# Kernel optimization log

Hardware: AMD Instinct MI355X
Metric: run time of the kernel (lower is better)

Reference implementation:

```python
import jax, jax.numpy as jnp
import numpy as np

B, S, H, D = 4, 1024, 16, 128
E = H * D  # 2048
TOTAL = B * S
NUM_SLOTS = 2 * TOTAL


def setup_inputs() -> dict:
    key = jax.random.key(0)
    k1, k2, k3, k4, k5 = jax.random.split(key, 5)
    return {
        "hidden_states": jax.random.normal(k1, (TOTAL, E), dtype=jnp.float32) * 0.02,
        "c_attn_w": jax.random.normal(k2, (E, 3 * E), dtype=jnp.float32) * 0.02,
        "c_attn_b": jax.random.normal(k3, (3 * E,), dtype=jnp.float32) * 0.02,
        "c_proj_w": jax.random.normal(k4, (E, E), dtype=jnp.float32) * 0.02,
        "c_proj_b": jax.random.normal(k5, (E,), dtype=jnp.float32) * 0.02,
        "key_cache": jnp.zeros((NUM_SLOTS, H, D), dtype=jnp.float32),
        "value_cache": jnp.zeros((NUM_SLOTS, H, D), dtype=jnp.float32),
        "slots": jnp.arange(TOTAL, dtype=jnp.int32),
        "seq_len": S,
    }


def reference(hidden_states, c_attn_w, c_attn_b, c_proj_w, c_proj_b,
              key_cache, value_cache, slots, seq_len):
    total, embed = hidden_states.shape
    n_heads, head_dim = key_cache.shape[1], key_cache.shape[2]
    b = total // seq_len

    # fused QKV projection (fan_in_fan_out: y = x @ W + b)
    qkv = hidden_states @ c_attn_w + c_attn_b            # [total, 3E]
    qkv = qkv.reshape(total, 3, n_heads, head_dim)
    q, k, v = qkv[:, 0], qkv[:, 1], qkv[:, 2]

    # paged_attention.reshape_and_cache: scatter new k/v into the paged cache
    key_cache = key_cache.at[slots].set(k)
    value_cache = value_cache.at[slots].set(v)
    # prefill attention reads current tokens' k/v (gathered back from cache)
    k = key_cache[slots]
    v = value_cache[slots]

    # varlen causal flash attention over b equal-length sequences
    qb = q.reshape(b, seq_len, n_heads, head_dim)
    kb = k.reshape(b, seq_len, n_heads, head_dim)
    vb = v.reshape(b, seq_len, n_heads, head_dim)
    scale = jnp.asarray(head_dim, qb.dtype) ** -0.5       # softmax_scale
    scores = jnp.einsum("bqhd,bkhd->bhqk", qb, kb) * scale
    causal = jnp.tril(jnp.ones((seq_len, seq_len), dtype=bool))
    scores = jnp.where(causal, scores, jnp.finfo(scores.dtype).min)
    attn = jax.nn.softmax(scores, axis=-1)
    ctx = jnp.einsum("bhqk,bkhd->bqhd", attn, vb)
    ctx = ctx.reshape(total, embed)

    # output projection (fan_in_fan_out row-parallel linear)
    out = ctx @ c_proj_w + c_proj_b
    return out
```

## Files before the change

kernel.cpp:

```cpp
#include <hip/hip_runtime.h>
#include <stdint.h>

typedef __bf16 bf16x8 __attribute__((ext_vector_type(8)));
typedef float  f32x4  __attribute__((ext_vector_type(4)));

#define DEV static __device__ __forceinline__

DEV unsigned short f2bf(float x) {
    union { float f; unsigned int u; } v; v.f = x;
    unsigned int r = v.u + 0x7FFFu + ((v.u >> 16) & 1u);
    return (unsigned short)(r >> 16);
}

DEV void gl_lds16(const void* g, void* l) {
    __builtin_amdgcn_global_load_lds(
        (__attribute__((address_space(1))) void*)(g),
        (__attribute__((address_space(3))) void*)(l), 16, 0, 0);
}

DEV f32x4 zero4() { f32x4 z; z[0]=0.f; z[1]=0.f; z[2]=0.f; z[3]=0.f; return z; }

__global__ void k_cvt_bf16(const float* __restrict__ in, unsigned short* __restrict__ out, int n) {
    int i = (blockIdx.x * blockDim.x + threadIdx.x) * 4;
    int stride = gridDim.x * blockDim.x * 4;
    for (; i < n; i += stride) {
        float4 f = *(const float4*)(in + i);
        ushort4 o;
        o.x = f2bf(f.x); o.y = f2bf(f.y); o.z = f2bf(f.z); o.w = f2bf(f.w);
        *(ushort4*)(out + i) = o;
    }
}

__global__ void k_transpose_bf16(const float* __restrict__ in, unsigned short* __restrict__ out,
                                 int K, int N) {
    __shared__ float tile[32][33];
    int n0 = blockIdx.x * 32, k0 = blockIdx.y * 32;
    int tx = threadIdx.x, ty = threadIdx.y;
    #pragma unroll
    for (int i = 0; i < 4; i++)
        tile[ty + i*8][tx] = in[(size_t)(k0 + ty + i*8) * N + n0 + tx];
    __syncthreads();
    #pragma unroll
    for (int i = 0; i < 4; i++)
        out[(size_t)(n0 + ty + i*8) * K + k0 + tx] = f2bf(tile[tx][ty + i*8]);
}

template<int MODE>
__launch_bounds__(256, 4)
__global__ void k_gemm(const unsigned short* __restrict__ A,
                       const unsigned short* __restrict__ BT,
                       const float* __restrict__ bias,
                       float* __restrict__ outp,
                       unsigned short* __restrict__ q_buf,
                       unsigned short* __restrict__ k_buf,
                       unsigned short* __restrict__ vt_buf,
                       int M, int N, int K) {
    __shared__ __align__(16) uint4 As[128*8];
    __shared__ __align__(16) uint4 Bs[128*8];

    const int t = threadIdx.x;
    const int wave = t >> 6, lane = t & 63, quad = lane >> 4, l15 = lane & 15;
    const int wm = wave & 1, wn = wave >> 1;
    const int bm = blockIdx.x, bn = blockIdx.y;

    f32x4 acc[4][4];
    #pragma unroll
    for (int i = 0; i < 4; i++)
        #pragma unroll
        for (int j = 0; j < 4; j++) acc[i][j] = zero4();

    int rS[4], gS[4];
    #pragma unroll
    for (int p = 0; p < 4; p++) {
        int c = p*4 + wave;
        int s = c*64 + lane;
        int r = s >> 3;
        rS[p] = r; gS[p] = (lane & 7) ^ (r & 7);
    }
    const unsigned short* Abase = A  + (size_t)(bm*128) * K;
    const unsigned short* Bbase = BT + (size_t)(bn*128) * K;

    const int kiters = K >> 6;
    for (int kk = 0; kk < kiters; kk++) {
        const int k0 = kk * 64;
        __syncthreads();
        #pragma unroll
        for (int p = 0; p < 4; p++) {
            int c = p*4 + wave;
            gl_lds16(Abase + (size_t)rS[p]*K + k0 + gS[p]*8, &As[c*64]);
            gl_lds16(Bbase + (size_t)rS[p]*K + k0 + gS[p]*8, &Bs[c*64]);
        }
        __syncthreads();
        #pragma unroll
        for (int ks = 0; ks < 2; ks++) {
            bf16x8 af[4], bfr[4];
            #pragma unroll
            for (int mt = 0; mt < 4; mt++) {
                int row = wm*64 + mt*16 + l15;
                int g = (ks*4 + quad) ^ (row & 7);
                af[mt] = __builtin_bit_cast(bf16x8, As[row*8 + g]);
            }
            #pragma unroll
            for (int nt = 0; nt < 4; nt++) {
                int row = wn*64 + nt*16 + l15;
                int g = (ks*4 + quad) ^ (row & 7);
                bfr[nt] = __builtin_bit_cast(bf16x8, Bs[row*8 + g]);
            }
            #pragma unroll
            for (int mt = 0; mt < 4; mt++)
                #pragma unroll
                for (int nt = 0; nt < 4; nt++)
                    acc[mt][nt] = __builtin_amdgcn_mfma_f32_16x16x32_bf16(
                        af[mt], bfr[nt], acc[mt][nt], 0, 0, 0);
        }
    }

    if (MODE == 1) {
        #pragma unroll
        for (int nt = 0; nt < 4; nt++) {
            int n = bn*128 + wn*64 + nt*16 + l15;
            float bv = bias[n];
            #pragma unroll
            for (int mt = 0; mt < 4; mt++) {
                int m = bm*128 + wm*64 + mt*16 + quad*4;
                #pragma unroll
                for (int r = 0; r < 4; r++)
                    outp[(size_t)(m + r) * N + n] = acc[mt][nt][r] + bv;
            }
        }
    } else {
        const int nglob = bn * 128;
        const int seg = nglob >> 11;
        const int cn_base = (nglob & 2047) + wn*64;
        if (seg < 2) {
            unsigned short* dst = (seg == 0) ? q_buf : k_buf;
            const float scl = (seg == 0) ? 0.08838834764831845f : 1.0f;
            #pragma unroll
            for (int nt = 0; nt < 4; nt++) {
                int cn = cn_base + nt*16 + l15;
                float bv = bias[nglob + wn*64 + nt*16 + l15];
                #pragma unroll
                for (int mt = 0; mt < 4; mt++) {
                    int tt = bm*128 + wm*64 + mt*16 + quad*4;
                    #pragma unroll
                    for (int r = 0; r < 4; r++)
                        dst[(size_t)(tt + r) * 2048 + cn] = f2bf((acc[mt][nt][r] + bv) * scl);
                }
            }
        } else {
            #pragma unroll
            for (int nt = 0; nt < 4; nt++) {
                int cn = cn_base + nt*16 + l15;
                int h = cn >> 7, d = cn & 127;
                float bv = bias[nglob + wn*64 + nt*16 + l15];
                #pragma unroll
                for (int mt = 0; mt < 4; mt++) {
                    int tt = bm*128 + wm*64 + mt*16 + quad*4;
                    int b = tt >> 10, s = tt & 1023;
                    ushort4 pk;
                    pk.x = f2bf(acc[mt][nt][0] + bv);
                    pk.y = f2bf(acc[mt][nt][1] + bv);
                    pk.z = f2bf(acc[mt][nt][2] + bv);
                    pk.w = f2bf(acc[mt][nt][3] + bv);
                    *(ushort4*)(vt_buf + ((size_t)((b*16 + h)*128 + d) * 1024 + s)) = pk;
                }
            }
        }
    }
}

#define ATTN_ITEMS 512
__launch_bounds__(256, 2)
__global__ void k_attn(const unsigned short* __restrict__ q_buf,
                       const unsigned short* __restrict__ k_buf,
                       const unsigned short* __restrict__ vt_buf,
                       unsigned short* __restrict__ ctx_buf,
                       int* __restrict__ counter) {
    __shared__ __align__(16) uint4 Ks[64*16];
    __shared__ __align__(16) uint4 Vs[128*8];
    __shared__ __align__(16) unsigned short Pl[4][32*64];
    __shared__ int sh_item;

    const int t = threadIdx.x;
    const int wave = t >> 6, lane = t & 63, quad = lane >> 4, l15 = lane & 15;

    for (;;) {
        if (t == 0) sh_item = atomicAdd(counter, 1);
        __syncthreads();
        const int u = sh_item;
        if (u >= ATTN_ITEMS) break;
        const int qt = 7 - (u >> 6);
        const int bh = u & 63;
        const int b = bh >> 4, h = bh & 15;

        bf16x8 qf[2][4];
        #pragma unroll
        for (int rt = 0; rt < 2; rt++) {
            const size_t qoff = (size_t)(b*1024 + qt*128 + wave*32 + rt*16 + l15) * 2048 + h*128;
            #pragma unroll
            for (int ks = 0; ks < 4; ks++)
                qf[rt][ks] = __builtin_bit_cast(bf16x8, *(const uint4*)(q_buf + qoff + ks*32 + quad*8));
        }

        f32x4 ctx[2][8];
        #pragma unroll
        for (int rt = 0; rt < 2; rt++)
            #pragma unroll
            for (int i = 0; i < 8; i++) ctx[rt][i] = zero4();
        float l_run[2][4];
        #pragma unroll
        for (int rt = 0; rt < 2; rt++)
            #pragma unroll
            for (int r = 0; r < 4; r++) l_run[rt][r] = 0.f;

        const size_t kbase = (size_t)b * 1024 * 2048 + h*128;
        const size_t vbase = (size_t)(b*16 + h) * 131072;
        const int row0 = qt*128 + wave*32;

        const int kiters = 2*qt + 2;
        for (int kt = 0; kt < kiters; kt++) {
            __syncthreads();
            #pragma unroll
            for (int p = 0; p < 4; p++) {
                int c = p*4 + wave;
                {
                    int s = c*64 + lane;
                    int r = s >> 4;
                    int g = (s & 15) ^ (r & 15);
                    gl_lds16(k_buf + kbase + (size_t)(kt*64 + r) * 2048 + g*8, &Ks[c*64]);
                }
                {
                    int s = c*64 + lane;
                    int r = s >> 3;
                    int g = (lane & 7) ^ (r & 7);
                    gl_lds16(vt_buf + vbase + (size_t)r * 1024 + kt*64 + g*8, &Vs[c*64]);
                }
            }
            __syncthreads();

            if (kt*64 > row0 + 31) continue;
            const bool needmask = (kt*64 + 63 > row0);

            #pragma unroll
            for (int rt = 0; rt < 2; rt++) {
                f32x4 sacc[4];
                #pragma unroll
                for (int nt = 0; nt < 4; nt++) sacc[nt] = zero4();
                #pragma unroll
                for (int ks = 0; ks < 4; ks++)
                    #pragma unroll
                    for (int nt = 0; nt < 4; nt++) {
                        int key = nt*16 + l15;
                        int g = (ks*4 + quad) ^ (key & 15);
                        bf16x8 kf = __builtin_bit_cast(bf16x8, Ks[key*16 + g]);
                        sacc[nt] = __builtin_amdgcn_mfma_f32_16x16x32_bf16(qf[rt][ks], kf, sacc[nt], 0, 0, 0);
                    }

                float pv[4][4];
                if (needmask) {
                    #pragma unroll
                    for (int nt = 0; nt < 4; nt++)
                        #pragma unroll
                        for (int r = 0; r < 4; r++) {
                            bool masked = (kt*64 + nt*16 + l15 > row0 + rt*16 + quad*4 + r);
                            pv[nt][r] = masked ? 0.f : __expf(sacc[nt][r]);
                        }
                } else {
                    #pragma unroll
                    for (int nt = 0; nt < 4; nt++)
                        #pragma unroll
                        for (int r = 0; r < 4; r++)
                            pv[nt][r] = __expf(sacc[nt][r]);
                }
                #pragma unroll
                for (int r = 0; r < 4; r++)
                    l_run[rt][r] += (pv[0][r] + pv[1][r]) + (pv[2][r] + pv[3][r]);

                #pragma unroll
                for (int nt = 0; nt < 4; nt++)
                    #pragma unroll
                    for (int r = 0; r < 4; r++) {
                        int row = rt*16 + quad*4 + r;
                        int col = nt*16 + l15;
                        int gc = (col >> 3) ^ (row & 7);
                        Pl[wave][row*64 + gc*8 + (col & 7)] = f2bf(pv[nt][r]);
                    }
            }
            __asm__ volatile("s_waitcnt lgkmcnt(0)" ::: "memory");

            #pragma unroll
            for (int rt = 0; rt < 2; rt++)
                #pragma unroll
                for (int ks = 0; ks < 2; ks++) {
                    int row = rt*16 + l15;
                    int gp = (ks*4 + quad) ^ (row & 7);
                    bf16x8 pa = __builtin_bit_cast(bf16x8, *(const uint4*)&Pl[wave][row*64 + gp*8]);
                    #pragma unroll
                    for (int dt = 0; dt < 8; dt++) {
                        int drow = dt*16 + l15;
                        int gv = (ks*4 + quad) ^ (drow & 7);
                        bf16x8 vf = __builtin_bit_cast(bf16x8, Vs[drow*8 + gv]);
                        ctx[rt][dt] = __builtin_amdgcn_mfma_f32_16x16x32_bf16(pa, vf, ctx[rt][dt], 0, 0, 0);
                    }
                }
        }

        #pragma unroll
        for (int rt = 0; rt < 2; rt++) {
            float inv[4];
            #pragma unroll
            for (int r = 0; r < 4; r++) {
                float l = l_run[rt][r];
                l += __shfl_xor(l, 1);
                l += __shfl_xor(l, 2);
                l += __shfl_xor(l, 4);
                l += __shfl_xor(l, 8);
                inv[r] = 1.0f / l;
            }
            const int tt0 = b*1024 + qt*128 + wave*32 + rt*16 + quad*4;
            #pragma unroll
            for (int dt = 0; dt < 8; dt++)
                #pragma unroll
                for (int r = 0; r < 4; r++)
                    ctx_buf[(size_t)(tt0 + r) * 2048 + h*128 + dt*16 + l15] = f2bf(ctx[rt][dt][r] * inv[r]);
        }
    }
}

extern "C" void kernel_launch(void* const* d_in, const int* in_sizes, int n_in,
                              void* d_out, int out_size, void* d_ws, size_t ws_size,
                              hipStream_t stream) {
    const float* hs    = (const float*)d_in[0];
    const float* wqkv  = (const float*)d_in[1];
    const float* bqkv  = (const float*)d_in[2];
    const float* wproj = (const float*)d_in[3];
    const float* bproj = (const float*)d_in[4];

    char* ws = (char*)d_ws;
    unsigned short* hs_bf   = (unsigned short*)(ws);
    unsigned short* wqkvT   = (unsigned short*)(ws + 16777216ull);
    unsigned short* wprojT  = (unsigned short*)(ws + 41943040ull);
    unsigned short* q_buf   = (unsigned short*)(ws + 50331648ull);
    unsigned short* k_buf   = (unsigned short*)(ws + 67108864ull);
    unsigned short* vt_buf  = (unsigned short*)(ws + 83886080ull);
    unsigned short* ctx_buf = (unsigned short*)(ws + 100663296ull);
    int* counter = (int*)ws;

    k_cvt_bf16<<<2048, 256, 0, stream>>>(hs, hs_bf, 4096 * 2048);
    k_transpose_bf16<<<dim3(6144/32, 2048/32), dim3(32, 8), 0, stream>>>(wqkv, wqkvT, 2048, 6144);
    k_transpose_bf16<<<dim3(2048/32, 2048/32), dim3(32, 8), 0, stream>>>(wproj, wprojT, 2048, 2048);

    k_gemm<0><<<dim3(32, 48), 256, 0, stream>>>(hs_bf, wqkvT, bqkv, nullptr,
                                                q_buf, k_buf, vt_buf, 4096, 6144, 2048);
    hipMemsetAsync(counter, 0, 4, stream);
    k_attn<<<dim3(448), 256, 0, stream>>>(q_buf, k_buf, vt_buf, ctx_buf, counter);
    k_gemm<1><<<dim3(32, 16), 256, 0, stream>>>(ctx_buf, wprojT, bproj, (float*)d_out,
                                                nullptr, nullptr, nullptr, 4096, 2048, 2048);
}
```

Before: 392.3 us.

## Split projection GEMM into 64-row tiles and interleave attention MFMAs

```diff
diff --git a/kernel.cpp b/kernel.cpp
--- a/kernel.cpp
+++ b/kernel.cpp
@@ -45,16 +45,14 @@
         out[(size_t)(n0 + ty + i*8) * K + k0 + tx] = f2bf(tile[tx][ty + i*8]);
 }
 
-template<int MODE>
 __launch_bounds__(256, 4)
-__global__ void k_gemm(const unsigned short* __restrict__ A,
-                       const unsigned short* __restrict__ BT,
-                       const float* __restrict__ bias,
-                       float* __restrict__ outp,
-                       unsigned short* __restrict__ q_buf,
-                       unsigned short* __restrict__ k_buf,
-                       unsigned short* __restrict__ vt_buf,
-                       int M, int N, int K) {
+__global__ void k_gemm_qkv(const unsigned short* __restrict__ A,
+                           const unsigned short* __restrict__ BT,
+                           const float* __restrict__ bias,
+                           unsigned short* __restrict__ q_buf,
+                           unsigned short* __restrict__ k_buf,
+                           unsigned short* __restrict__ vt_buf,
+                           int K) {
     __shared__ __align__(16) uint4 As[128*8];
     __shared__ __align__(16) uint4 Bs[128*8];
 
@@ -115,62 +113,128 @@
         }
     }
 
-    if (MODE == 1) {
+    const int nglob = bn * 128;
+    const int seg = nglob >> 11;
+    const int cn_base = (nglob & 2047) + wn*64;
+    if (seg < 2) {
+        unsigned short* dst = (seg == 0) ? q_buf : k_buf;
+        const float scl = (seg == 0) ? 0.08838834764831845f : 1.0f;
         #pragma unroll
         for (int nt = 0; nt < 4; nt++) {
-            int n = bn*128 + wn*64 + nt*16 + l15;
-            float bv = bias[n];
+            int cn = cn_base + nt*16 + l15;
+            float bv = bias[nglob + wn*64 + nt*16 + l15];
             #pragma unroll
             for (int mt = 0; mt < 4; mt++) {
-                int m = bm*128 + wm*64 + mt*16 + quad*4;
+                int tt = bm*128 + wm*64 + mt*16 + quad*4;
                 #pragma unroll
                 for (int r = 0; r < 4; r++)
-                    outp[(size_t)(m + r) * N + n] = acc[mt][nt][r] + bv;
+                    dst[(size_t)(tt + r) * 2048 + cn] = f2bf((acc[mt][nt][r] + bv) * scl);
             }
         }
     } else {
-        const int nglob = bn * 128;
-        const int seg = nglob >> 11;
-        const int cn_base = (nglob & 2047) + wn*64;
-        if (seg < 2) {
-            unsigned short* dst = (seg == 0) ? q_buf : k_buf;
-            const float scl = (seg == 0) ? 0.08838834764831845f : 1.0f;
+        #pragma unroll
+        for (int nt = 0; nt < 4; nt++) {
+            int cn = cn_base + nt*16 + l15;
+            int h = cn >> 7, d = cn & 127;
+            float bv = bias[nglob + wn*64 + nt*16 + l15];
+            #pragma unroll
+            for (int mt = 0; mt < 4; mt++) {
+                int tt = bm*128 + wm*64 + mt*16 + quad*4;
+                int b = tt >> 10, s = tt & 1023;
+                ushort4 pk;
+                pk.x = f2bf(acc[mt][nt][0] + bv);
+                pk.y = f2bf(acc[mt][nt][1] + bv);
+                pk.z = f2bf(acc[mt][nt][2] + bv);
+                pk.w = f2bf(acc[mt][nt][3] + bv);
+                *(ushort4*)(vt_buf + ((size_t)((b*16 + h)*128 + d) * 1024 + s)) = pk;
+            }
+        }
+    }
+}
+
+__launch_bounds__(256, 4)
+__global__ void k_gemm_proj(const unsigned short* __restrict__ A,
+                            const unsigned short* __restrict__ BT,
+                            const float* __restrict__ bias,
+                            float* __restrict__ outp,
+                            int N, int K) {
+    __shared__ __align__(16) uint4 As[64*8];
+    __shared__ __align__(16) uint4 Bs[128*8];
+
+    const int t = threadIdx.x;
+    const int wave = t >> 6, lane = t & 63, quad = lane >> 4, l15 = lane & 15;
+    const int wm = wave & 1, wn = wave >> 1;
+    const int bm = blockIdx.x, bn = blockIdx.y;
+
+    f32x4 acc[2][4];
+    #pragma unroll
+    for (int i = 0; i < 2; i++)
+        #pragma unroll
+        for (int j = 0; j < 4; j++) acc[i][j] = zero4();
+
+    int rS[4], gS[4];
+    #pragma unroll
+    for (int p = 0; p < 4; p++) {
+        int c = p*4 + wave;
+        int s = c*64 + lane;
+        int r = s >> 3;
+        rS[p] = r; gS[p] = (lane & 7) ^ (r & 7);
+    }
+    const unsigned short* Abase = A  + (size_t)(bm*64)  * K;
+    const unsigned short* Bbase = BT + (size_t)(bn*128) * K;
+
+    const int kiters = K >> 6;
+    for (int kk = 0; kk < kiters; kk++) {
+        const int k0 = kk * 64;
+        __syncthreads();
+        #pragma unroll
+        for (int p = 0; p < 4; p++) {
+            int c = p*4 + wave;
+            if (p < 2)
+                gl_lds16(Abase + (size_t)rS[p]*K + k0 + gS[p]*8, &As[c*64]);
+            gl_lds16(Bbase + (size_t)rS[p]*K + k0 + gS[p]*8, &Bs[c*64]);
+        }
+        __syncthreads();
+        #pragma unroll
+        for (int ks = 0; ks < 2; ks++) {
+            bf16x8 af[2], bfr[4];
+            #pragma unroll
+            for (int mt = 0; mt < 2; mt++) {
+                int row = wm*32 + mt*16 + l15;
+                int g = (ks*4 + quad) ^ (row & 7);
+                af[mt] = __builtin_bit_cast(bf16x8, As[row*8 + g]);
+            }
             #pragma unroll
             for (int nt = 0; nt < 4; nt++) {
-                int cn = cn_base + nt*16 + l15;
-                float bv = bias[nglob + wn*64 + nt*16 + l15];
-                #pragma unroll
-                for (int mt = 0; mt < 4; mt++) {
-                    int tt = bm*128 + wm*64 + mt*16 + quad*4;
-                    #pragma unroll
-                    for (int r = 0; r < 4; r++)
-                        dst[(size_t)(tt + r) * 2048 + cn] = f2bf((acc[mt][nt][r] + bv) * scl);
-                }
-            }
-        } else {
-            #pragma unroll
-            for (int nt = 0; nt < 4; nt++) {
-                int cn = cn_base + nt*16 + l15;
-                int h = cn >> 7, d = cn & 127;
-                float bv = bias[nglob + wn*64 + nt*16 + l15];
-                #pragma unroll
-                for (int mt = 0; mt < 4; mt++) {
-                    int tt = bm*128 + wm*64 + mt*16 + quad*4;
-                    int b = tt >> 10, s = tt & 1023;
-                    ushort4 pk;
-                    pk.x = f2bf(acc[mt][nt][0] + bv);
-                    pk.y = f2bf(acc[mt][nt][1] + bv);
-                    pk.z = f2bf(acc[mt][nt][2] + bv);
-                    pk.w = f2bf(acc[mt][nt][3] + bv);
-                    *(ushort4*)(vt_buf + ((size_t)((b*16 + h)*128 + d) * 1024 + s)) = pk;
-                }
-            }
+                int row = wn*64 + nt*16 + l15;
+                int g = (ks*4 + quad) ^ (row & 7);
+                bfr[nt] = __builtin_bit_cast(bf16x8, Bs[row*8 + g]);
+            }
+            #pragma unroll
+            for (int mt = 0; mt < 2; mt++)
+                #pragma unroll
+                for (int nt = 0; nt < 4; nt++)
+                    acc[mt][nt] = __builtin_amdgcn_mfma_f32_16x16x32_bf16(
+                        af[mt], bfr[nt], acc[mt][nt], 0, 0, 0);
+        }
+    }
+
+    #pragma unroll
+    for (int nt = 0; nt < 4; nt++) {
+        int n = bn*128 + wn*64 + nt*16 + l15;
+        float bv = bias[n];
+        #pragma unroll
+        for (int mt = 0; mt < 2; mt++) {
+            int m = bm*64 + wm*32 + mt*16 + quad*4;
+            #pragma unroll
+            for (int r = 0; r < 4; r++)
+                outp[(size_t)(m + r) * N + n] = acc[mt][nt][r] + bv;
         }
     }
 }
 
 #define ATTN_ITEMS 512
-__launch_bounds__(256, 2)
+__launch_bounds__(256, 3)
 __global__ void k_attn(const unsigned short* __restrict__ q_buf,
                        const unsigned short* __restrict__ k_buf,
                        const unsigned short* __restrict__ vt_buf,
@@ -241,21 +305,24 @@
             if (kt*64 > row0 + 31) continue;
             const bool needmask = (kt*64 + 63 > row0);
 
+            f32x4 sacc[2][4];
+            #pragma unroll
+            for (int rt = 0; rt < 2; rt++)
+                #pragma unroll
+                for (int nt = 0; nt < 4; nt++) sacc[rt][nt] = zero4();
+            #pragma unroll
+            for (int ks = 0; ks < 4; ks++)
+                #pragma unroll
+                for (int nt = 0; nt < 4; nt++) {
+                    int key = nt*16 + l15;
+                    int g = (ks*4 + quad) ^ (key & 15);
+                    bf16x8 kf = __builtin_bit_cast(bf16x8, Ks[key*16 + g]);
+                    sacc[0][nt] = __builtin_amdgcn_mfma_f32_16x16x32_bf16(qf[0][ks], kf, sacc[0][nt], 0, 0, 0);
+                    sacc[1][nt] = __builtin_amdgcn_mfma_f32_16x16x32_bf16(qf[1][ks], kf, sacc[1][nt], 0, 0, 0);
+                }
+
             #pragma unroll
             for (int rt = 0; rt < 2; rt++) {
-                f32x4 sacc[4];
-                #pragma unroll
-                for (int nt = 0; nt < 4; nt++) sacc[nt] = zero4();
-                #pragma unroll
-                for (int ks = 0; ks < 4; ks++)
-                    #pragma unroll
-                    for (int nt = 0; nt < 4; nt++) {
-                        int key = nt*16 + l15;
-                        int g = (ks*4 + quad) ^ (key & 15);
-                        bf16x8 kf = __builtin_bit_cast(bf16x8, Ks[key*16 + g]);
-                        sacc[nt] = __builtin_amdgcn_mfma_f32_16x16x32_bf16(qf[rt][ks], kf, sacc[nt], 0, 0, 0);
-                    }
-
                 float pv[4][4];
                 if (needmask) {
                     #pragma unroll
@@ -263,14 +330,14 @@
                         #pragma unroll
                         for (int r = 0; r < 4; r++) {
                             bool masked = (kt*64 + nt*16 + l15 > row0 + rt*16 + quad*4 + r);
-                            pv[nt][r] = masked ? 0.f : __expf(sacc[nt][r]);
+                            pv[nt][r] = masked ? 0.f : __expf(sacc[rt][nt][r]);
                         }
                 } else {
                     #pragma unroll
                     for (int nt = 0; nt < 4; nt++)
                         #pragma unroll
                         for (int r = 0; r < 4; r++)
-                            pv[nt][r] = __expf(sacc[nt][r]);
+                            pv[nt][r] = __expf(sacc[rt][nt][r]);
                 }
                 #pragma unroll
                 for (int r = 0; r < 4; r++)
@@ -289,20 +356,23 @@
             __asm__ volatile("s_waitcnt lgkmcnt(0)" ::: "memory");
 
             #pragma unroll
-            for (int rt = 0; rt < 2; rt++)
-                #pragma unroll
-                for (int ks = 0; ks < 2; ks++) {
+            for (int ks = 0; ks < 2; ks++) {
+                bf16x8 pa[2];
+                #pragma unroll
+                for (int rt = 0; rt < 2; rt++) {
                     int row = rt*16 + l15;
                     int gp = (ks*4 + quad) ^ (row & 7);
-                    bf16x8 pa = __builtin_bit_cast(bf16x8, *(const uint4*)&Pl[wave][row*64 + gp*8]);
-                    #pragma unroll
-                    for (int dt = 0; dt < 8; dt++) {
-                        int drow = dt*16 + l15;
-                        int gv = (ks*4 + quad) ^ (drow & 7);
-                        bf16x8 vf = __builtin_bit_cast(bf16x8, Vs[drow*8 + gv]);
-                        ctx[rt][dt] = __builtin_amdgcn_mfma_f32_16x16x32_bf16(pa, vf, ctx[rt][dt], 0, 0, 0);
-                    }
-                }
+                    pa[rt] = __builtin_bit_cast(bf16x8, *(const uint4*)&Pl[wave][row*64 + gp*8]);
+                }
+                #pragma unroll
+                for (int dt = 0; dt < 8; dt++) {
+                    int drow = dt*16 + l15;
+                    int gv = (ks*4 + quad) ^ (drow & 7);
+                    bf16x8 vf = __builtin_bit_cast(bf16x8, Vs[drow*8 + gv]);
+                    ctx[0][dt] = __builtin_amdgcn_mfma_f32_16x16x32_bf16(pa[0], vf, ctx[0][dt], 0, 0, 0);
+                    ctx[1][dt] = __builtin_amdgcn_mfma_f32_16x16x32_bf16(pa[1], vf, ctx[1][dt], 0, 0, 0);
+                }
+            }
         }
 
         #pragma unroll
@@ -350,10 +420,8 @@
     k_transpose_bf16<<<dim3(6144/32, 2048/32), dim3(32, 8), 0, stream>>>(wqkv, wqkvT, 2048, 6144);
     k_transpose_bf16<<<dim3(2048/32, 2048/32), dim3(32, 8), 0, stream>>>(wproj, wprojT, 2048, 2048);
 
-    k_gemm<0><<<dim3(32, 48), 256, 0, stream>>>(hs_bf, wqkvT, bqkv, nullptr,
-                                                q_buf, k_buf, vt_buf, 4096, 6144, 2048);
+    k_gemm_qkv<<<dim3(32, 48), 256, 0, stream>>>(hs_bf, wqkvT, bqkv, q_buf, k_buf, vt_buf, 2048);
     hipMemsetAsync(counter, 0, 4, stream);
-    k_attn<<<dim3(448), 256, 0, stream>>>(q_buf, k_buf, vt_buf, ctx_buf, counter);
-    k_gemm<1><<<dim3(32, 16), 256, 0, stream>>>(ctx_buf, wprojT, bproj, (float*)d_out,
-                                                nullptr, nullptr, nullptr, 4096, 2048, 2048);
-}
+    k_attn<<<dim3(512), 256, 0, stream>>>(q_buf, k_buf, vt_buf, ctx_buf, counter);
+    k_gemm_proj<<<dim3(64, 16), 256, 0, stream>>>(ctx_buf, wprojT, bproj, (float*)d_out, 2048, 2048);
+}
```

Result: slower. 562.7 us (+43.4%).
